# Performance work log

Measured on AMD Instinct MI355X. Metric: run time of the kernel, lower is better.

## Reference

```python
import jax, jax.numpy as jnp
import numpy as np

GAMMA = 0.99
GAE_LAMBDA = 0.95
CLIP_PARAM = 0.2
VALUE_LOSS_COEF = 0.5
ENTROPY_COEF = 0.01
T, N = 1024, 8192

def setup_inputs() -> dict:
    key = jax.random.key(0)
    ks = jax.random.split(key, 9)
    rewards = jax.random.normal(ks[0], (T, N, 1), dtype=jnp.float32)
    masks = (jax.random.uniform(ks[1], (T + 1, N, 1)) > 0.02).astype(jnp.float32)
    bad_masks = (jax.random.uniform(ks[2], (T + 1, N, 1)) > 0.01).astype(jnp.float32)
    value_preds = jax.random.normal(ks[3], (T + 1, N, 1), dtype=jnp.float32)
    last_value = jax.random.normal(ks[4], (N, 1), dtype=jnp.float32)
    log_prob = jax.random.normal(ks[5], (T, N, 1), dtype=jnp.float32) * 0.1
    prev_log_prob = jax.random.normal(ks[6], (T, N, 1), dtype=jnp.float32) * 0.1
    new_value = jax.random.normal(ks[7], (T, N, 1), dtype=jnp.float32)
    dist_entropy = jax.random.normal(ks[8], (T, N, 1), dtype=jnp.float32)
    return {"rewards": rewards, "masks": masks, "bad_masks": bad_masks,
            "value_preds": value_preds, "last_value": last_value,
            "log_prob": log_prob, "prev_log_prob": prev_log_prob,
            "new_value": new_value, "dist_entropy": dist_entropy}


def _compute_derived(rewards, masks, bad_masks, value_preds, last_value):
    # value_preds is detached in the original update(); mirror with stop_gradient
    vp = jax.lax.stop_gradient(value_preds)
    lv = jax.lax.stop_gradient(last_value)
    vp = vp.at[-1].set(lv)  # value_preds[-1] = last_value

    def step(gae, xs):
        r, v_next, v, m_next, bad_next = xs
        delta = r + GAMMA * v_next * m_next - v
        gae = (delta + GAMMA * GAE_LAMBDA * m_next * gae) * bad_next
        return gae, gae + v  # returns[step] = gae + value_preds[step]

    xs = (rewards, vp[1:], vp[:-1], masks[1:], bad_masks[1:])
    init = jnp.zeros_like(lv)
    _, returns_t = jax.lax.scan(step, init, xs, reverse=True)  # (T, N, 1)

    advantages = returns_t - vp[:-1]
    advantages = (advantages - advantages.mean()) / (advantages.std(ddof=1) + 1e-5)
    return advantages, returns_t


def reference(rewards, masks, bad_masks, value_preds, last_value,
              log_prob, prev_log_prob, new_value, dist_entropy):
    advantages, returns_t = _compute_derived(rewards, masks, bad_masks,
                                             value_preds, last_value)
    # PPO clipped surrogate (single minibatch = full rollout, flattened over T*N)
    ratio = jnp.exp(log_prob - prev_log_prob)
    surr1 = ratio * advantages
    surr2 = jnp.clip(ratio, 1.0 - CLIP_PARAM, 1.0 + CLIP_PARAM) * advantages
    action_loss = -jnp.minimum(surr1, surr2).mean()

    value_target = jax.lax.stop_gradient(returns_t)
    old_value = jax.lax.stop_gradient(value_preds[:-1])
    value_pred_clipped = old_value + jnp.clip(new_value - old_value,
                                              -CLIP_PARAM, CLIP_PARAM)
    value_losses = (new_value - value_target) ** 2
    value_losses_clipped = (value_pred_clipped - value_target) ** 2
    value_loss = 0.5 * jnp.maximum(value_losses, value_losses_clipped).mean()

    loss = (value_loss * VALUE_LOSS_COEF + action_loss
            - dist_entropy.mean() * ENTROPY_COEF)
    return loss
```

## Files before the change

kernel.cpp:

```cpp
#include <hip/hip_runtime.h>
#include <math.h>

#define T_DIM 1024
#define N_DIM 8192
#define M_TOT (T_DIM * N_DIM)
#define NVEC  (M_TOT / 4)
#define NV4   (N_DIM / 4)
#define L_CHUNK 8
#define C_CHUNKS 128

#define PC_BLOCKS   ((C_CHUNKS * NV4) / 256)
#define LOSS_BLOCKS 2048
#define LOSS_STRIDE (LOSS_BLOCKS * 256)

#define kGAMMA 0.99f
#define kGLAM  (0.99f * 0.95f)


__device__ __forceinline__ unsigned short f2bf(float f) {
    unsigned int u = __float_as_uint(f);
    u += 0x7fffu + ((u >> 16) & 1u);
    return (unsigned short)(u >> 16);
}
__device__ __forceinline__ float bf2f(unsigned short h) {
    return __uint_as_float(((unsigned int)h) << 16);
}

__global__ __launch_bounds__(256) void k_pc(
    const float4* __restrict__ r4,
    const float4* __restrict__ m4,
    const float4* __restrict__ bm4,
    const float4* __restrict__ vp4,
    const float4* __restrict__ lv4,
    ushort4* __restrict__ b16,
    float4* __restrict__ A_out,
    float4* __restrict__ B_out)
{
    const int g  = blockIdx.x * 256 + threadIdx.x;
    const int j  = g & (NV4 - 1);
    const int c  = g >> 11;
    const int t0 = c * L_CHUNK;

    float4 vnext = (c == C_CHUNKS - 1) ? lv4[j] : vp4[(t0 + L_CHUNK) * NV4 + j];
    float4 Aa = make_float4(1.f, 1.f, 1.f, 1.f);
    float4 Bb = make_float4(0.f, 0.f, 0.f, 0.f);

    #pragma unroll
    for (int i = L_CHUNK - 1; i >= 0; --i) {
        const int idx = (t0 + i) * NV4 + j;
        const float4 r  = r4[idx];
        const float4 v  = vp4[idx];
        const float4 m  = m4[idx + NV4];
        const float4 bb = bm4[idx + NV4];

        ushort4 o;
        {
            const float b = (fmaf(kGAMMA * m.x, vnext.x, r.x) - v.x) * bb.x;
            const float a = kGLAM * m.x * bb.x;
            Aa.x = a * Aa.x; Bb.x = fmaf(a, Bb.x, b);
            o.x = (unsigned short)((f2bf(b) & 0xFFFEu) | ((m.x * bb.x > 0.5f) ? 1u : 0u));
        }
        {
            const float b = (fmaf(kGAMMA * m.y, vnext.y, r.y) - v.y) * bb.y;
            const float a = kGLAM * m.y * bb.y;
            Aa.y = a * Aa.y; Bb.y = fmaf(a, Bb.y, b);
            o.y = (unsigned short)((f2bf(b) & 0xFFFEu) | ((m.y * bb.y > 0.5f) ? 1u : 0u));
        }
        {
            const float b = (fmaf(kGAMMA * m.z, vnext.z, r.z) - v.z) * bb.z;
            const float a = kGLAM * m.z * bb.z;
            Aa.z = a * Aa.z; Bb.z = fmaf(a, Bb.z, b);
            o.z = (unsigned short)((f2bf(b) & 0xFFFEu) | ((m.z * bb.z > 0.5f) ? 1u : 0u));
        }
        {
            const float b = (fmaf(kGAMMA * m.w, vnext.w, r.w) - v.w) * bb.w;
            const float a = kGLAM * m.w * bb.w;
            Aa.w = a * Aa.w; Bb.w = fmaf(a, Bb.w, b);
            o.w = (unsigned short)((f2bf(b) & 0xFFFEu) | ((m.w * bb.w > 0.5f) ? 1u : 0u));
        }
        b16[idx] = o;
        vnext = v;
    }
    A_out[c * NV4 + j] = Aa;
    B_out[c * NV4 + j] = Bb;
}

__global__ __launch_bounds__(256) void k_ginc(
    const float* __restrict__ A_in,
    const float* __restrict__ B_in,
    float* __restrict__ g_in)
{
    const int n = blockIdx.x * 256 + threadIdx.x;
    float g = 0.0f;
    constexpr int PB = 16;
    for (int cb = C_CHUNKS - PB; cb >= 0; cb -= PB) {
        float Ar[PB], Br[PB];
        #pragma unroll
        for (int i = 0; i < PB; ++i) {
            Ar[i] = A_in[(cb + i) * N_DIM + n];
            Br[i] = B_in[(cb + i) * N_DIM + n];
        }
        #pragma unroll
        for (int i = PB - 1; i >= 0; --i) {
            g_in[(cb + i) * N_DIM + n] = g;
            g = fmaf(Ar[i], g, Br[i]);
        }
    }
}

__device__ __forceinline__ void gae_comp(float& gae, unsigned short h,
                                         float v, float nvv,
                                         float& sg, float& sg2, float& v_s) {
    const float bf = bf2f(h);
    const float a  = (h & 1u) ? kGLAM : 0.0f;
    gae = fmaf(a, gae, bf);
    sg += gae;
    sg2 = fmaf(gae, gae, sg2);
    const float q  = nvv - v;
    const float e1 = q - gae;
    const float e2 = fminf(fmaxf(q, -0.2f), 0.2f) - gae;
    v_s += fmaxf(e1 * e1, e2 * e2);
}

__global__ __launch_bounds__(256) void k_gae(
    ushort4* __restrict__ bg16,
    const float4* __restrict__ g_in4,
    const float4* __restrict__ vp4,
    const float4* __restrict__ nv4,
    double* __restrict__ pg)
{
    const int g  = blockIdx.x * 256 + threadIdx.x;
    const int j  = g & (NV4 - 1);
    const int c  = g >> 11;
    const int t0 = c * L_CHUNK;

    float4 gae = g_in4[c * NV4 + j];
    float sg = 0.f, sg2 = 0.f, v_s = 0.f;

    #pragma unroll
    for (int i = L_CHUNK - 1; i >= 0; --i) {
        const int idx = (t0 + i) * NV4 + j;
        const ushort4 h = bg16[idx];
        const float4  v = vp4[idx];
        const float4  q = nv4[idx];
        gae_comp(gae.x, h.x, v.x, q.x, sg, sg2, v_s);
        gae_comp(gae.y, h.y, v.y, q.y, sg, sg2, v_s);
        gae_comp(gae.z, h.z, v.z, q.z, sg, sg2, v_s);
        gae_comp(gae.w, h.w, v.w, q.w, sg, sg2, v_s);
        ushort4 o;
        o.x = f2bf(gae.x); o.y = f2bf(gae.y); o.z = f2bf(gae.z); o.w = f2bf(gae.w);
        bg16[idx] = o;
    }

    double d0 = (double)sg, d1 = (double)sg2, d2 = (double)v_s;
    #pragma unroll
    for (int off = 32; off > 0; off >>= 1) {
        d0 += __shfl_down(d0, off, 64);
        d1 += __shfl_down(d1, off, 64);
        d2 += __shfl_down(d2, off, 64);
    }
    __shared__ double sh[3][4];
    const int wid = threadIdx.x >> 6, lane = threadIdx.x & 63;
    if (lane == 0) { sh[0][wid] = d0; sh[1][wid] = d1; sh[2][wid] = d2; }
    __syncthreads();
    if (threadIdx.x == 0) {
        double t0s = 0, t1s = 0, t2s = 0;
        #pragma unroll
        for (int w = 0; w < 4; ++w) { t0s += sh[0][w]; t1s += sh[1][w]; t2s += sh[2][w]; }
        pg[blockIdx.x * 3 + 0] = t0s;
        pg[blockIdx.x * 3 + 1] = t1s;
        pg[blockIdx.x * 3 + 2] = t2s;
    }
}

__global__ __launch_bounds__(256) void k_stats(
    const double* __restrict__ pg, double* __restrict__ acc)
{
    double s0 = 0.0, s1 = 0.0, s2 = 0.0;
    for (int i = threadIdx.x; i < PC_BLOCKS; i += 256) {
        s0 += pg[i * 3 + 0];
        s1 += pg[i * 3 + 1];
        s2 += pg[i * 3 + 2];
    }
    #pragma unroll
    for (int off = 32; off > 0; off >>= 1) {
        s0 += __shfl_down(s0, off, 64);
        s1 += __shfl_down(s1, off, 64);
        s2 += __shfl_down(s2, off, 64);
    }
    __shared__ double sh[3][4];
    const int wid = threadIdx.x >> 6, lane = threadIdx.x & 63;
    if (lane == 0) { sh[0][wid] = s0; sh[1][wid] = s1; sh[2][wid] = s2; }
    __syncthreads();
    if (threadIdx.x == 0) {
        double sum = 0, sum2 = 0, vsum = 0;
        #pragma unroll
        for (int w = 0; w < 4; ++w) { sum += sh[0][w]; sum2 += sh[1][w]; vsum += sh[2][w]; }
        const double M = (double)M_TOT;
        const double mu = sum / M;
        double var = (sum2 - sum * sum / M) / (M - 1.0);
        if (var < 0.0) var = 0.0;
        acc[3] = vsum;
        acc[5] = mu;
        acc[6] = 1.0 / (sqrt(var) + 1e-5);
    }
}

__global__ __launch_bounds__(256) void k_loss(
    const ushort4* __restrict__ gae16,
    const float4* __restrict__ lp4,
    const float4* __restrict__ plp4,
    const float4* __restrict__ ent4,
    const double* __restrict__ acc,
    double* __restrict__ pl)
{
    const int tid = blockIdx.x * 256 + threadIdx.x;
    const float mu   = (float)acc[5];
    const float invs = (float)acc[6];

    float a_s = 0.f, e_s = 0.f;
    #pragma unroll
    for (int k = 0; k < 4; ++k) {
        const int i = tid + k * LOSS_STRIDE;
        const ushort4 G = gae16[i];
        const float4  L = lp4[i];
        const float4  P = plp4[i];
        const float4  E = ent4[i];
        const float gs[4] = {bf2f(G.x), bf2f(G.y), bf2f(G.z), bf2f(G.w)};
        const float ls[4] = {L.x, L.y, L.z, L.w};
        const float ps[4] = {P.x, P.y, P.z, P.w};
        #pragma unroll
        for (int c = 0; c < 4; ++c) {
            const float x  = (gs[c] - mu) * invs;
            const float r  = __expf(ls[c] - ps[c]);
            const float rc = fminf(fmaxf(r, 0.8f), 1.2f);
            a_s += fminf(r * x, rc * x);
        }
        e_s += E.x + E.y + E.z + E.w;
    }

    double d0 = (double)a_s, d1 = (double)e_s;
    #pragma unroll
    for (int off = 32; off > 0; off >>= 1) {
        d0 += __shfl_down(d0, off, 64);
        d1 += __shfl_down(d1, off, 64);
    }
    __shared__ double sh[2][4];
    const int wid = threadIdx.x >> 6, lane = threadIdx.x & 63;
    if (lane == 0) { sh[0][wid] = d0; sh[1][wid] = d1; }
    __syncthreads();
    if (threadIdx.x == 0) {
        double t0s = 0, t1s = 0;
        #pragma unroll
        for (int w = 0; w < 4; ++w) { t0s += sh[0][w]; t1s += sh[1][w]; }
        pl[blockIdx.x * 2 + 0] = t0s;
        pl[blockIdx.x * 2 + 1] = t1s;
    }
}

__global__ __launch_bounds__(256) void k_final(
    const double* __restrict__ pl, const double* __restrict__ acc,
    float* __restrict__ out)
{
    double s0 = 0.0, s1 = 0.0;
    for (int i = threadIdx.x; i < LOSS_BLOCKS; i += 256) {
        s0 += pl[i * 2 + 0];
        s1 += pl[i * 2 + 1];
    }
    #pragma unroll
    for (int off = 32; off > 0; off >>= 1) {
        s0 += __shfl_down(s0, off, 64);
        s1 += __shfl_down(s1, off, 64);
    }
    __shared__ double sh[2][4];
    const int wid = threadIdx.x >> 6, lane = threadIdx.x & 63;
    if (lane == 0) { sh[0][wid] = s0; sh[1][wid] = s1; }
    __syncthreads();
    if (threadIdx.x == 0) {
        double a_sum = 0, e_sum = 0;
        #pragma unroll
        for (int w = 0; w < 4; ++w) { a_sum += sh[0][w]; e_sum += sh[1][w]; }
        const double M = (double)M_TOT;
        out[0] = (float)(0.25 * acc[3] / M - a_sum / M - 0.01 * e_sum / M);
    }
}

extern "C" void kernel_launch(void* const* d_in, const int* in_sizes, int n_in,
                              void* d_out, int out_size, void* d_ws, size_t ws_size,
                              hipStream_t stream) {
    const float* rewards     = (const float*)d_in[0];
    const float* masks       = (const float*)d_in[1];
    const float* bad_masks   = (const float*)d_in[2];
    const float* value_preds = (const float*)d_in[3];
    const float* last_value  = (const float*)d_in[4];
    const float* log_prob    = (const float*)d_in[5];
    const float* prev_lp     = (const float*)d_in[6];
    const float* new_value   = (const float*)d_in[7];
    const float* dist_ent    = (const float*)d_in[8];

    char* ws = (char*)d_ws;
    double* acc = (double*)ws;
    double* pg  = (double*)(ws + 256);
    double* pl  = (double*)(ws + 32768);
    unsigned short* b16 = (unsigned short*)(ws + 65536);
    float* A = (float*)(ws + 65536 + (size_t)M_TOT * 2);
    float* B = (float*)(ws + 65536 + (size_t)M_TOT * 2 + (size_t)C_CHUNKS * N_DIM * 4);

    k_pc<<<PC_BLOCKS, 256, 0, stream>>>((const float4*)rewards,
                                        (const float4*)masks,
                                        (const float4*)bad_masks,
                                        (const float4*)value_preds,
                                        (const float4*)last_value,
                                        (ushort4*)b16, (float4*)A, (float4*)B);
    k_ginc<<<N_DIM / 256, 256, 0, stream>>>(A, B, A );
    k_gae<<<PC_BLOCKS, 256, 0, stream>>>((ushort4*)b16,
                                         (const float4*)A ,
                                         (const float4*)value_preds,
                                         (const float4*)new_value, pg);
    k_stats<<<1, 256, 0, stream>>>(pg, acc);
    k_loss<<<LOSS_BLOCKS, 256, 0, stream>>>((const ushort4*)b16 ,
                                            (const float4*)log_prob,
                                            (const float4*)prev_lp,
                                            (const float4*)dist_ent, acc, pl);
    k_final<<<1, 256, 0, stream>>>(pl, acc, (float*)d_out);
}
```

Baseline: 273.6 us.

## Parallelize carry scan across chunks and recompute GAE in loss kernel

Replaces the serial per-column carry pass (32 blocks walking 128 chunks) with a parallel scan where 16 lanes each compose 8 chunk affine maps and combine them with shuffles, which exposes far more parallelism. The GAE kernel no longer writes bf16 GAE back; instead the loss kernel recomputes GAE from the packed deltas and chunk carries. This removes a full-size write and the separate stats kernel, since each loss block re-reduces the partial sums itself. In exchange the loss kernel rereads b16 and the carries, and every block redundantly reduces the 1024 partial sums.

Result: no change. 269.5 us (-1.5%).

```diff
diff --git a/kernel.cpp b/kernel.cpp
--- a/kernel.cpp
+++ b/kernel.cpp
@@ -4,14 +4,11 @@
 #define T_DIM 1024
 #define N_DIM 8192
 #define M_TOT (T_DIM * N_DIM)
-#define NVEC  (M_TOT / 4)
 #define NV4   (N_DIM / 4)
 #define L_CHUNK 8
-#define C_CHUNKS 128
-
-#define PC_BLOCKS   ((C_CHUNKS * NV4) / 256)
-#define LOSS_BLOCKS 2048
-#define LOSS_STRIDE (LOSS_BLOCKS * 256)
+#define C_CHUNKS (T_DIM / L_CHUNK)
+#define PC_BLOCKS ((C_CHUNKS * NV4) / 256)
+#define SCAN_BLOCKS ((NV4 * 16) / 256)
 
 #define kGAMMA 0.99f
 #define kGLAM  (0.99f * 0.95f)
@@ -85,26 +82,54 @@
     B_out[c * NV4 + j] = Bb;
 }
 
-__global__ __launch_bounds__(256) void k_ginc(
-    const float* __restrict__ A_in,
-    const float* __restrict__ B_in,
-    float* __restrict__ g_in)
-{
-    const int n = blockIdx.x * 256 + threadIdx.x;
-    float g = 0.0f;
-    constexpr int PB = 16;
-    for (int cb = C_CHUNKS - PB; cb >= 0; cb -= PB) {
-        float Ar[PB], Br[PB];
-        #pragma unroll
-        for (int i = 0; i < PB; ++i) {
-            Ar[i] = A_in[(cb + i) * N_DIM + n];
-            Br[i] = B_in[(cb + i) * N_DIM + n];
-        }
-        #pragma unroll
-        for (int i = PB - 1; i >= 0; --i) {
-            g_in[(cb + i) * N_DIM + n] = g;
-            g = fmaf(Ar[i], g, Br[i]);
-        }
+__global__ __launch_bounds__(256) void k_scan(
+    float4* __restrict__ Ag,
+    const float4* __restrict__ Bg)
+{
+    const int u  = blockIdx.x * 256 + threadIdx.x;
+    const int jj = u >> 4;
+    const int k  = u & 15;
+
+    float4 As[8], Bs[8];
+    #pragma unroll
+    for (int i = 0; i < 8; ++i) {
+        As[i] = Ag[(8 * k + i) * NV4 + jj];
+        Bs[i] = Bg[(8 * k + i) * NV4 + jj];
+    }
+    float4 Pa = As[7], Pb = Bs[7];
+    #pragma unroll
+    for (int i = 6; i >= 0; --i) {
+        Pb.x = fmaf(As[i].x, Pb.x, Bs[i].x); Pa.x = As[i].x * Pa.x;
+        Pb.y = fmaf(As[i].y, Pb.y, Bs[i].y); Pa.y = As[i].y * Pa.y;
+        Pb.z = fmaf(As[i].z, Pb.z, Bs[i].z); Pa.z = As[i].z * Pa.z;
+        Pb.w = fmaf(As[i].w, Pb.w, Bs[i].w); Pa.w = As[i].w * Pa.w;
+    }
+    #pragma unroll
+    for (int d = 1; d < 16; d <<= 1) {
+        const float nax = __shfl_down(Pa.x, d, 16), nay = __shfl_down(Pa.y, d, 16);
+        const float naz = __shfl_down(Pa.z, d, 16), naw = __shfl_down(Pa.w, d, 16);
+        const float nbx = __shfl_down(Pb.x, d, 16), nby = __shfl_down(Pb.y, d, 16);
+        const float nbz = __shfl_down(Pb.z, d, 16), nbw = __shfl_down(Pb.w, d, 16);
+        if (k + d < 16) {
+            Pb.x = fmaf(Pa.x, nbx, Pb.x); Pa.x *= nax;
+            Pb.y = fmaf(Pa.y, nby, Pb.y); Pa.y *= nay;
+            Pb.z = fmaf(Pa.z, nbz, Pb.z); Pa.z *= naz;
+            Pb.w = fmaf(Pa.w, nbw, Pb.w); Pa.w *= naw;
+        }
+    }
+    float4 G;
+    G.x = __shfl_down(Pb.x, 1, 16);
+    G.y = __shfl_down(Pb.y, 1, 16);
+    G.z = __shfl_down(Pb.z, 1, 16);
+    G.w = __shfl_down(Pb.w, 1, 16);
+    if (k == 15) G = make_float4(0.f, 0.f, 0.f, 0.f);
+    #pragma unroll
+    for (int i = 7; i >= 0; --i) {
+        Ag[(8 * k + i) * NV4 + jj] = G;
+        G.x = fmaf(As[i].x, G.x, Bs[i].x);
+        G.y = fmaf(As[i].y, G.y, Bs[i].y);
+        G.z = fmaf(As[i].z, G.z, Bs[i].z);
+        G.w = fmaf(As[i].w, G.w, Bs[i].w);
     }
 }
 
@@ -123,7 +148,7 @@
 }
 
 __global__ __launch_bounds__(256) void k_gae(
-    ushort4* __restrict__ bg16,
+    const ushort4* __restrict__ b16,
     const float4* __restrict__ g_in4,
     const float4* __restrict__ vp4,
     const float4* __restrict__ nv4,
@@ -140,16 +165,13 @@
     #pragma unroll
     for (int i = L_CHUNK - 1; i >= 0; --i) {
         const int idx = (t0 + i) * NV4 + j;
-        const ushort4 h = bg16[idx];
+        const ushort4 h = b16[idx];
         const float4  v = vp4[idx];
         const float4  q = nv4[idx];
         gae_comp(gae.x, h.x, v.x, q.x, sg, sg2, v_s);
         gae_comp(gae.y, h.y, v.y, q.y, sg, sg2, v_s);
         gae_comp(gae.z, h.z, v.z, q.z, sg, sg2, v_s);
         gae_comp(gae.w, h.w, v.w, q.w, sg, sg2, v_s);
-        ushort4 o;
-        o.x = f2bf(gae.x); o.y = f2bf(gae.y); o.z = f2bf(gae.z); o.w = f2bf(gae.w);
-        bg16[idx] = o;
     }
 
     double d0 = (double)sg, d1 = (double)sg2, d2 = (double)v_s;
@@ -173,13 +195,104 @@
     }
 }
 
-__global__ __launch_bounds__(256) void k_stats(
-    const double* __restrict__ pg, double* __restrict__ acc)
+__global__ __launch_bounds__(256) void k_loss(
+    const ushort4* __restrict__ b16,
+    const float4* __restrict__ g_in4,
+    const float4* __restrict__ lp4,
+    const float4* __restrict__ plp4,
+    const float4* __restrict__ ent4,
+    const double* __restrict__ pg,
+    double* __restrict__ pl)
+{
+    __shared__ double sh[3][4];
+    __shared__ double bc[2];
+    const int tid = threadIdx.x;
+
+    {
+        double s0 = 0.0, s1 = 0.0;
+        for (int i = tid; i < PC_BLOCKS; i += 256) {
+            s0 += pg[i * 3 + 0];
+            s1 += pg[i * 3 + 1];
+        }
+        #pragma unroll
+        for (int off = 32; off > 0; off >>= 1) {
+            s0 += __shfl_down(s0, off, 64);
+            s1 += __shfl_down(s1, off, 64);
+        }
+        const int wid = tid >> 6, lane = tid & 63;
+        if (lane == 0) { sh[0][wid] = s0; sh[1][wid] = s1; }
+        __syncthreads();
+        if (tid == 0) {
+            double sum = 0, sum2 = 0;
+            #pragma unroll
+            for (int w = 0; w < 4; ++w) { sum += sh[0][w]; sum2 += sh[1][w]; }
+            const double M = (double)M_TOT;
+            const double mu = sum / M;
+            double var = (sum2 - sum * sum / M) / (M - 1.0);
+            if (var < 0.0) var = 0.0;
+            bc[0] = mu;
+            bc[1] = 1.0 / (sqrt(var) + 1e-5);
+        }
+        __syncthreads();
+    }
+    const float mu   = (float)bc[0];
+    const float invs = (float)bc[1];
+
+    const int g  = blockIdx.x * 256 + tid;
+    const int j  = g & (NV4 - 1);
+    const int c  = g >> 11;
+    const int t0 = c * L_CHUNK;
+
+    float4 gv = g_in4[c * NV4 + j];
+    float a_s = 0.f, e_s = 0.f;
+
+    #pragma unroll
+    for (int i = L_CHUNK - 1; i >= 0; --i) {
+        const int idx = (t0 + i) * NV4 + j;
+        const ushort4 h = b16[idx];
+        const float4 Lp = lp4[idx];
+        const float4 Pp = plp4[idx];
+        const float4 E  = ent4[idx];
+#define P5C(comp, H) { \
+        const unsigned short hh = (H); \
+        const float bf = bf2f(hh); \
+        const float a  = (hh & 1u) ? kGLAM : 0.0f; \
+        gv.comp = fmaf(a, gv.comp, bf); \
+        const float x  = (gv.comp - mu) * invs; \
+        const float rr = __expf(Lp.comp - Pp.comp); \
+        const float rc = fminf(fmaxf(rr, 0.8f), 1.2f); \
+        a_s += fminf(rr * x, rc * x); }
+        P5C(x, h.x) P5C(y, h.y) P5C(z, h.z) P5C(w, h.w)
+#undef P5C
+        e_s += E.x + E.y + E.z + E.w;
+    }
+
+    double d0 = (double)a_s, d1 = (double)e_s;
+    #pragma unroll
+    for (int off = 32; off > 0; off >>= 1) {
+        d0 += __shfl_down(d0, off, 64);
+        d1 += __shfl_down(d1, off, 64);
+    }
+    const int wid = tid >> 6, lane = tid & 63;
+    if (lane == 0) { sh[0][wid] = d0; sh[1][wid] = d1; }
+    __syncthreads();
+    if (tid == 0) {
+        double t0s = 0, t1s = 0;
+        #pragma unroll
+        for (int w = 0; w < 4; ++w) { t0s += sh[0][w]; t1s += sh[1][w]; }
+        pl[blockIdx.x * 2 + 0] = t0s;
+        pl[blockIdx.x * 2 + 1] = t1s;
+    }
+}
+
+__global__ __launch_bounds__(256) void k_final(
+    const double* __restrict__ pg, const double* __restrict__ pl,
+    float* __restrict__ out)
 {
     double s0 = 0.0, s1 = 0.0, s2 = 0.0;
     for (int i = threadIdx.x; i < PC_BLOCKS; i += 256) {
-        s0 += pg[i * 3 + 0];
-        s1 += pg[i * 3 + 1];
+        s0 += pl[i * 2 + 0];
+        s1 += pl[i * 2 + 1];
         s2 += pg[i * 3 + 2];
     }
     #pragma unroll
@@ -193,95 +306,11 @@
     if (lane == 0) { sh[0][wid] = s0; sh[1][wid] = s1; sh[2][wid] = s2; }
     __syncthreads();
     if (threadIdx.x == 0) {
-        double sum = 0, sum2 = 0, vsum = 0;
+        double a_sum = 0, e_sum = 0, vsum = 0;
         #pragma unroll
-        for (int w = 0; w < 4; ++w) { sum += sh[0][w]; sum2 += sh[1][w]; vsum += sh[2][w]; }
+        for (int w = 0; w < 4; ++w) { a_sum += sh[0][w]; e_sum += sh[1][w]; vsum += sh[2][w]; }
         const double M = (double)M_TOT;
-        const double mu = sum / M;
-        double var = (sum2 - sum * sum / M) / (M - 1.0);
-        if (var < 0.0) var = 0.0;
-        acc[3] = vsum;
-        acc[5] = mu;
-        acc[6] = 1.0 / (sqrt(var) + 1e-5);
-    }
-}
-
-__global__ __launch_bounds__(256) void k_loss(
-    const ushort4* __restrict__ gae16,
-    const float4* __restrict__ lp4,
-    const float4* __restrict__ plp4,
-    const float4* __restrict__ ent4,
-    const double* __restrict__ acc,
-    double* __restrict__ pl)
-{
-    const int tid = blockIdx.x * 256 + threadIdx.x;
-    const float mu   = (float)acc[5];
-    const float invs = (float)acc[6];
-
-    float a_s = 0.f, e_s = 0.f;
-    #pragma unroll
-    for (int k = 0; k < 4; ++k) {
-        const int i = tid + k * LOSS_STRIDE;
-        const ushort4 G = gae16[i];
-        const float4  L = lp4[i];
-        const float4  P = plp4[i];
-        const float4  E = ent4[i];
-        const float gs[4] = {bf2f(G.x), bf2f(G.y), bf2f(G.z), bf2f(G.w)};
-        const float ls[4] = {L.x, L.y, L.z, L.w};
-        const float ps[4] = {P.x, P.y, P.z, P.w};
-        #pragma unroll
-        for (int c = 0; c < 4; ++c) {
-            const float x  = (gs[c] - mu) * invs;
-            const float r  = __expf(ls[c] - ps[c]);
-            const float rc = fminf(fmaxf(r, 0.8f), 1.2f);
-            a_s += fminf(r * x, rc * x);
-        }
-        e_s += E.x + E.y + E.z + E.w;
-    }
-
-    double d0 = (double)a_s, d1 = (double)e_s;
-    #pragma unroll
-    for (int off = 32; off > 0; off >>= 1) {
-        d0 += __shfl_down(d0, off, 64);
-        d1 += __shfl_down(d1, off, 64);
-    }
-    __shared__ double sh[2][4];
-    const int wid = threadIdx.x >> 6, lane = threadIdx.x & 63;
-    if (lane == 0) { sh[0][wid] = d0; sh[1][wid] = d1; }
-    __syncthreads();
-    if (threadIdx.x == 0) {
-        double t0s = 0, t1s = 0;
-        #pragma unroll
-        for (int w = 0; w < 4; ++w) { t0s += sh[0][w]; t1s += sh[1][w]; }
-        pl[blockIdx.x * 2 + 0] = t0s;
-        pl[blockIdx.x * 2 + 1] = t1s;
-    }
-}
-
-__global__ __launch_bounds__(256) void k_final(
-    const double* __restrict__ pl, const double* __restrict__ acc,
-    float* __restrict__ out)
-{
-    double s0 = 0.0, s1 = 0.0;
-    for (int i = threadIdx.x; i < LOSS_BLOCKS; i += 256) {
-        s0 += pl[i * 2 + 0];
-        s1 += pl[i * 2 + 1];
-    }
-    #pragma unroll
-    for (int off = 32; off > 0; off >>= 1) {
-        s0 += __shfl_down(s0, off, 64);
-        s1 += __shfl_down(s1, off, 64);
-    }
-    __shared__ double sh[2][4];
-    const int wid = threadIdx.x >> 6, lane = threadIdx.x & 63;
-    if (lane == 0) { sh[0][wid] = s0; sh[1][wid] = s1; }
-    __syncthreads();
-    if (threadIdx.x == 0) {
-        double a_sum = 0, e_sum = 0;
-        #pragma unroll
-        for (int w = 0; w < 4; ++w) { a_sum += sh[0][w]; e_sum += sh[1][w]; }
-        const double M = (double)M_TOT;
-        out[0] = (float)(0.25 * acc[3] / M - a_sum / M - 0.01 * e_sum / M);
+        out[0] = (float)(0.25 * vsum / M - a_sum / M - 0.01 * e_sum / M);
     }
 }
 
@@ -299,7 +328,6 @@
     const float* dist_ent    = (const float*)d_in[8];
 
     char* ws = (char*)d_ws;
-    double* acc = (double*)ws;
     double* pg  = (double*)(ws + 256);
     double* pl  = (double*)(ws + 32768);
     unsigned short* b16 = (unsigned short*)(ws + 65536);
@@ -312,15 +340,15 @@
                                         (const float4*)value_preds,
                                         (const float4*)last_value,
                                         (ushort4*)b16, (float4*)A, (float4*)B);
-    k_ginc<<<N_DIM / 256, 256, 0, stream>>>(A, B, A );
-    k_gae<<<PC_BLOCKS, 256, 0, stream>>>((ushort4*)b16,
+    k_scan<<<SCAN_BLOCKS, 256, 0, stream>>>((float4*)A, (const float4*)B);
+    k_gae<<<PC_BLOCKS, 256, 0, stream>>>((const ushort4*)b16,
                                          (const float4*)A ,
                                          (const float4*)value_preds,
                                          (const float4*)new_value, pg);
-    k_stats<<<1, 256, 0, stream>>>(pg, acc);
-    k_loss<<<LOSS_BLOCKS, 256, 0, stream>>>((const ushort4*)b16 ,
-                                            (const float4*)log_prob,
-                                            (const float4*)prev_lp,
-                                            (const float4*)dist_ent, acc, pl);
-    k_final<<<1, 256, 0, stream>>>(pl, acc, (float*)d_out);
-}
+    k_loss<<<PC_BLOCKS, 256, 0, stream>>>((const ushort4*)b16,
+                                          (const float4*)A ,
+                                          (const float4*)log_prob,
+                                          (const float4*)prev_lp,
+                                          (const float4*)dist_ent, pg, pl);
+    k_final<<<1, 256, 0, stream>>>(pg, pl, (float*)d_out);
+}
```
